# Performance work log

Measured on AMD Instinct MI355X. Metric: run time of the kernel, lower is better.

The kernel has to match this reference:

```python
import jax, jax.numpy as jnp
import numpy as np

M_IND = 1024   # inducing points
K_NN = 16      # nearest neighbors
JITTER = 1e-4


def rbf(X, Z):
    # unit-variance, unit-lengthscale RBF kernel; returns (K, squared distances)
    sq = jnp.sum(X * X, -1)[:, None] + jnp.sum(Z * Z, -1)[None, :] - 2.0 * (X @ Z.T)
    sq = jnp.maximum(sq, 0.0)
    return jnp.exp(-0.5 * sq), sq


def setup_inputs() -> dict:
    key = jax.random.key(0)
    k1, k2, k3 = jax.random.split(key, 3)
    return {
        "X": jax.random.normal(k1, (65536, 3), jnp.float32),
        "Z": jax.random.normal(k2, (M_IND, 3), jnp.float32),
        "Lu_raw": jax.random.normal(k3, (M_IND, M_IND), jnp.float32),
        "mu": jnp.zeros((M_IND,), jnp.float32),
    }


def reference(X, Z, Lu_raw, mu):
    N = X.shape[0]
    Kxx = jnp.ones((N,), X.dtype)                      # diag of RBF(X,X) is 1
    Kxz, dist = rbf(X, Z)                              # [N,M], [N,M]
    Kzz, _ = rbf(Z, Z)                                 # [M,M]

    # transform_to(lower_cholesky): strict lower triangle + exp(diag)
    Lu = jnp.tril(Lu_raw, -1) + jnp.diag(jnp.exp(jnp.diag(Lu_raw)))

    eyeM = jnp.eye(M_IND, dtype=X.dtype)
    L = jnp.linalg.cholesky(Kzz + JITTER * eyeM)       # [M,M]
    Kzz_j = L @ L.T                                    # == little_L @ little_L.T math (Kzz + jitter*I)
    Su = Lu @ Lu.T                                     # full variational covariance

    # K nearest inducing points per data point (argsort(dist)[:, :K])
    _, idx = jax.lax.top_k(-dist, K_NN)                # [N,K]

    lKzz = Kzz_j[idx[:, :, None], idx[:, None, :]]     # [N,K,K] gathered submatrices
    lS = Su[idx[:, :, None], idx[:, None, :]]          # [N,K,K]
    lKxz = jnp.take_along_axis(Kxz, idx, axis=1)       # [N,K]
    lmu = mu[idx]                                      # [N,K]

    eyeK = jnp.eye(K_NN, dtype=X.dtype)
    inv = jnp.linalg.inv(lKzz + JITTER * eyeK)         # batched tiny inverses [N,K,K]
    W = jnp.einsum('nk,nkj->nj', lKxz, inv)            # [N,K]

    mean = jnp.einsum('nk,nk->n', W, lmu)              # [N]
    cov = (Kxx
           - jnp.einsum('ni,nij,nj->n', W, lKzz, W)
           + jnp.einsum('ni,nij,nj->n', W, lS, W))
    std = jnp.sqrt(jnp.clip(cov, 0.05, None))          # qF scale = clamp(cov, 0.05)**0.5
    return jnp.stack([mean, std])                      # [2,N] qF parameters
```

## Files before the change

### kernel.cpp

```cpp
#include <hip/hip_runtime.h>
#include <math.h>

#define N_PTS 65536
#define M_IND 1024
#define KNN 16
#define JITTER 1e-4f

#define PACKED_FLOATS (M_IND * (M_IND + 1) / 2)
#define PACKED_BYTES  ((size_t)PACKED_FLOATS * sizeof(float))

#define TSU 32
#define SU_BLOCKS 528
#define PTS_PER_BLK 128
#define QSTRIDE 17
#define GRID_BLKS (N_PTS / PTS_PER_BLK)

typedef float v2f __attribute__((ext_vector_type(2)));

__device__ __forceinline__ void su_tile(const float* __restrict__ Lu_raw,
                                        float* __restrict__ P,
                                        int bid, int tid,
                                        float (*As)[36], float (*Bs)[36]) {
    int rt = (int)((sqrtf(8.0f * (float)bid + 1.0f) - 1.0f) * 0.5f);
    while ((rt + 1) * (rt + 2) / 2 <= bid) ++rt;
    while (rt * (rt + 1) / 2 > bid) --rt;
    int ct = bid - rt * (rt + 1) / 2;
    int i0 = rt * TSU, j0 = ct * TSU;

    int tx = tid & 15, ty = tid >> 4;
    int sr = tid >> 3, sc = (tid & 7) << 2;
    float a00 = 0.f, a01 = 0.f, a10 = 0.f, a11 = 0.f;

    int nch = ct + 1;
    int gi = i0 + sr, gj = j0 + sr;
    float4 pa = *(const float4*)(Lu_raw + (unsigned)gi * M_IND + sc);
    float4 pb = *(const float4*)(Lu_raw + (unsigned)gj * M_IND + sc);

    for (int c = 0; c < nch; ++c) {
        int gk = (c << 5) + sc;
        float aa[4] = {pa.x, pa.y, pa.z, pa.w};
        float bb[4] = {pb.x, pb.y, pb.z, pb.w};
        #pragma unroll
        for (int q = 0; q < 4; ++q) {
            int k = gk + q;
            aa[q] = (k < gi) ? aa[q] : ((k == gi) ? __expf(aa[q]) : 0.0f);
            bb[q] = (k < gj) ? bb[q] : ((k == gj) ? __expf(bb[q]) : 0.0f);
        }
        *(float4*)&As[sr][sc] = make_float4(aa[0], aa[1], aa[2], aa[3]);
        *(float4*)&Bs[sr][sc] = make_float4(bb[0], bb[1], bb[2], bb[3]);
        __syncthreads();
        if (c + 1 < nch) {
            int kn = ((c + 1) << 5) + sc;
            pa = *(const float4*)(Lu_raw + (unsigned)gi * M_IND + kn);
            pb = *(const float4*)(Lu_raw + (unsigned)gj * M_IND + kn);
        }
        #pragma unroll
        for (int kk = 0; kk < 32; kk += 4) {
            float4 av0 = *(const float4*)&As[ty][kk];
            float4 av1 = *(const float4*)&As[ty + 16][kk];
            float4 bv0 = *(const float4*)&Bs[tx][kk];
            float4 bv1 = *(const float4*)&Bs[tx + 16][kk];
            a00 = fmaf(av0.x, bv0.x, fmaf(av0.y, bv0.y, fmaf(av0.z, bv0.z, fmaf(av0.w, bv0.w, a00))));
            a01 = fmaf(av0.x, bv1.x, fmaf(av0.y, bv1.y, fmaf(av0.z, bv1.z, fmaf(av0.w, bv1.w, a01))));
            a10 = fmaf(av1.x, bv0.x, fmaf(av1.y, bv0.y, fmaf(av1.z, bv0.z, fmaf(av1.w, bv0.w, a10))));
            a11 = fmaf(av1.x, bv1.x, fmaf(av1.y, bv1.y, fmaf(av1.z, bv1.z, fmaf(av1.w, bv1.w, a11))));
        }
        __syncthreads();
    }

    int ia = i0 + ty, ib = i0 + ty + 16;
    int ja = j0 + tx, jb = j0 + tx + 16;
    if (ja <= ia) P[((unsigned)ia * (ia + 1) >> 1) + ja] = a00;
    if (jb <= ia) P[((unsigned)ia * (ia + 1) >> 1) + jb] = a01;
    if (ja <= ib) P[((unsigned)ib * (ib + 1) >> 1) + ja] = a10;
    if (jb <= ib) P[((unsigned)ib * (ib + 1) >> 1) + jb] = a11;
}

__global__ __launch_bounds__(256) void su_kernel(const float* __restrict__ Lu_raw,
                                                 float* __restrict__ P) {
    __shared__ float As[TSU][36];
    __shared__ float Bs[TSU][36];
    su_tile(Lu_raw, P, blockIdx.x, threadIdx.x, As, Bs);
}

__device__ __forceinline__ void ce(unsigned long long& x, unsigned long long& y) {
    unsigned long long a = x, b = y;
    bool c = a < b;
    x = c ? a : b;
    y = c ? b : a;
}
__device__ __forceinline__ void ce(float& x, float& y) {
    float a = fminf(x, y), b = fmaxf(x, y);
    x = a; y = b;
}
__device__ __forceinline__ void ce(v2f& x, v2f& y) {
    v2f a = __builtin_elementwise_min(x, y);
    v2f b = __builtin_elementwise_max(x, y);
    x = a; y = b;
}

template <typename KT>
__device__ __forceinline__ void sort16(KT* a) {
    #pragma unroll
    for (int p = 1; p < 16; p <<= 1)
        #pragma unroll
        for (int k = p; k >= 1; k >>= 1)
            #pragma unroll
            for (int j = k & (p - 1); j + k < 16; j += 2 * k)
                #pragma unroll
                for (int i = 0; i < k; ++i)
                    if (i + j + k < 16)
                        if (((i + j) / (2 * p)) == ((i + j + k) / (2 * p)))
                            ce(a[i + j], a[i + j + k]);
}

template <typename KT>
__device__ __forceinline__ void cleanup16(KT* a) {
    #pragma unroll
    for (int d = 8; d >= 1; d >>= 1)
        #pragma unroll
        for (int i = 0; i < 16; ++i)
            if ((i & d) == 0) ce(a[i], a[i | d]);
}

__device__ __forceinline__ float distf(float4 z, float x0, float x1, float x2, float xq) {
    float dot = fmaf(x0, z.x, fmaf(x1, z.y, x2 * z.z));
    return fmaxf(fmaf(-2.0f, dot, xq + z.w), 0.0f);
}

__device__ __forceinline__ v2f dist2(float4 z, v2f x0, v2f x1, v2f x2, v2f xq) {
    v2f zx = {z.x, z.x}, zy = {z.y, z.y}, zz = {z.z, z.z}, zw = {z.w, z.w};
    v2f dot = __builtin_elementwise_fma(x0, zx,
              __builtin_elementwise_fma(x1, zy, x2 * zz));
    v2f d = __builtin_elementwise_fma((v2f){-2.0f, -2.0f}, dot, xq + zw);
    return __builtin_elementwise_max(d, (v2f){0.0f, 0.0f});
}

__device__ __forceinline__ v2f shfl_xor_v2f(v2f v, int mask) {
    unsigned long long u = __builtin_bit_cast(unsigned long long, v);
    u = __shfl_xor(u, mask, 64);
    return __builtin_bit_cast(v2f, u);
}

template <int MODE>
__global__ __launch_bounds__(256, 2) void vnngp_kernel(const float* __restrict__ X,
                                                       const float* __restrict__ Z,
                                                       const float* __restrict__ mu,
                                                       float* __restrict__ P,
                                                       const float* __restrict__ Lu_raw,
                                                       unsigned int* __restrict__ ctr,
                                                       float* __restrict__ out) {
    __shared__ __align__(16) char smem[37888];
    float4* Zs = (float4*)smem;
    float* mus = (float*)(smem + 16384);
    unsigned long long* qb = (unsigned long long*)(smem + 20480);
    int tid = threadIdx.x;

    for (int r = tid; r < M_IND; r += 256) {
        float zx = Z[r * 3 + 0], zy = Z[r * 3 + 1], zz = Z[r * 3 + 2];
        Zs[r] = make_float4(zx, zy, zz, zx * zx + zy * zy + zz * zz);
        mus[r] = mu[r];
    }

    if (MODE == 2) {
        float (*As)[36] = (float (*)[36])(smem + 20480);
        float (*Bs)[36] = (float (*)[36])(smem + 20480 + 4608);
        for (int t = blockIdx.x; t < SU_BLOCKS; t += GRID_BLKS)
            su_tile(Lu_raw, P, t, tid, As, Bs);
        __syncthreads();
        if (tid == 0) {
            __threadfence();
            atomicAdd(ctr, 1u);
        }
    } else {
        __syncthreads();
    }

    {
        int pt = tid >> 2, sub = tid & 3;
        int nA = blockIdx.x * PTS_PER_BLK + pt;
        int nB = nA + 64;
        float xA0 = X[nA * 3 + 0], xA1 = X[nA * 3 + 1], xA2 = X[nA * 3 + 2];
        float xB0 = X[nB * 3 + 0], xB1 = X[nB * 3 + 1], xB2 = X[nB * 3 + 2];
        v2f x0p = {xA0, xB0}, x1p = {xA1, xB1}, x2p = {xA2, xB2};
        v2f xqp = __builtin_elementwise_fma(x0p, x0p,
                  __builtin_elementwise_fma(x1p, x1p, x2p * x2p));
        int mbase = sub << 8;
        int rot = sub << 1;

        v2f T[16];
        #pragma unroll
        for (int j = 0; j < 16; ++j) T[j] = (v2f){3.4e38f, 3.4e38f};
        #pragma unroll 1
        for (int c = 0; c < 16; ++c) {
            int base = mbase + (c << 4);
            #pragma unroll
            for (int j = 0; j < 16; ++j) {
                int m = base + ((j + rot) & 15);
                v2f d = dist2(Zs[m], x0p, x1p, x2p, xqp);
                T[j] = __builtin_elementwise_min(T[j], d);
            }
        }
        sort16(T);
        #pragma unroll
        for (int round = 1; round <= 2; round <<= 1) {
            v2f o[16];
            #pragma unroll
            for (int i = 0; i < 16; ++i) o[i] = shfl_xor_v2f(T[i], round);
            #pragma unroll
            for (int i = 0; i < 16; ++i)
                T[i] = __builtin_elementwise_min(T[i], o[15 - i]);
            cleanup16(T);
        }
        v2f Tst = T[15];

        unsigned short* mycA = ((unsigned short*)qb) + pt * (QSTRIDE * 4) + sub * 16;
        unsigned short* mycB = ((unsigned short*)qb) + (pt + 64) * (QSTRIDE * 4) + sub * 16;
        int cntA = 0, cntB = 0;
        #pragma unroll 1
        for (int c = 0; c < 16; ++c) {
            int base = mbase + (c << 4);
            #pragma unroll
            for (int j = 0; j < 16; ++j) {
                int m = base + ((j + rot) & 15);
                v2f d = dist2(Zs[m], x0p, x1p, x2p, xqp);
                if (d.x <= Tst.x) { if (cntA < 16) mycA[cntA] = (unsigned short)m; ++cntA; }
                if (d.y <= Tst.y) { if (cntB < 16) mycB[cntB] = (unsigned short)m; ++cntB; }
            }
        }

        int ovfA = cntA > 16 ? 1 : 0;
        ovfA |= __shfl_xor(ovfA, 1, 64);
        ovfA |= __shfl_xor(ovfA, 2, 64);
        int ovfB = cntB > 16 ? 1 : 0;
        ovfB |= __shfl_xor(ovfB, 1, 64);
        ovfB |= __shfl_xor(ovfB, 2, 64);

        float xqA = xqp.x, xqB = xqp.y;

        if (!ovfA) {
            const unsigned long long* m64 = (const unsigned long long*)mycA;
            unsigned long long raw[4] = {m64[0], m64[1], m64[2], m64[3]};
            unsigned long long C[16];
            #pragma unroll
            for (int i = 0; i < 16; ++i) {
                int m = (int)((raw[i >> 2] >> ((i & 3) * 16)) & 0x3FF);
                float d = distf(Zs[m], xA0, xA1, xA2, xqA);
                unsigned long long key =
                    ((unsigned long long)__float_as_uint(d) << 32) | (unsigned)m;
                C[i] = (i < cntA) ? key : ~0ULL;
            }
            sort16(C);
            #pragma unroll
            for (int round = 1; round <= 2; round <<= 1) {
                unsigned long long o[16];
                #pragma unroll
                for (int i = 0; i < 16; ++i) o[i] = __shfl_xor(C[i], round, 64);
                #pragma unroll
                for (int i = 0; i < 16; ++i) {
                    unsigned long long b = o[15 - i];
                    C[i] = C[i] < b ? C[i] : b;
                }
                cleanup16(C);
            }
            if (sub == 0) {
                #pragma unroll
                for (int i = 0; i < 16; ++i) qb[pt * QSTRIDE + i] = C[i];
            }
        } else if (sub == 0) {
            unsigned long long R[16];
            #pragma unroll
            for (int i = 0; i < 16; ++i) R[i] = ~0ULL;
            for (int m = 0; m < M_IND; ++m) {
                float d = distf(Zs[m], xA0, xA1, xA2, xqA);
                unsigned long long kk =
                    ((unsigned long long)__float_as_uint(d) << 32) | (unsigned)m;
                if (kk < R[15]) {
                    #pragma unroll
                    for (int j = 0; j < 16; ++j) {
                        unsigned long long t = R[j];
                        bool cc = kk < t;
                        R[j] = cc ? kk : t;
                        kk = cc ? t : kk;
                    }
                }
            }
            #pragma unroll
            for (int i = 0; i < 16; ++i) qb[pt * QSTRIDE + i] = R[i];
        }

        if (!ovfB) {
            const unsigned long long* m64 = (const unsigned long long*)mycB;
            unsigned long long raw[4] = {m64[0], m64[1], m64[2], m64[3]};
            unsigned long long C[16];
            #pragma unroll
            for (int i = 0; i < 16; ++i) {
                int m = (int)((raw[i >> 2] >> ((i & 3) * 16)) & 0x3FF);
                float d = distf(Zs[m], xB0, xB1, xB2, xqB);
                unsigned long long key =
                    ((unsigned long long)__float_as_uint(d) << 32) | (unsigned)m;
                C[i] = (i < cntB) ? key : ~0ULL;
            }
            sort16(C);
            #pragma unroll
            for (int round = 1; round <= 2; round <<= 1) {
                unsigned long long o[16];
                #pragma unroll
                for (int i = 0; i < 16; ++i) o[i] = __shfl_xor(C[i], round, 64);
                #pragma unroll
                for (int i = 0; i < 16; ++i) {
                    unsigned long long b = o[15 - i];
                    C[i] = C[i] < b ? C[i] : b;
                }
                cleanup16(C);
            }
            if (sub == 0) {
                #pragma unroll
                for (int i = 0; i < 16; ++i) qb[(pt + 64) * QSTRIDE + i] = C[i];
            }
        } else if (sub == 0) {
            unsigned long long R[16];
            #pragma unroll
            for (int i = 0; i < 16; ++i) R[i] = ~0ULL;
            for (int m = 0; m < M_IND; ++m) {
                float d = distf(Zs[m], xB0, xB1, xB2, xqB);
                unsigned long long kk =
                    ((unsigned long long)__float_as_uint(d) << 32) | (unsigned)m;
                if (kk < R[15]) {
                    #pragma unroll
                    for (int j = 0; j < 16; ++j) {
                        unsigned long long t = R[j];
                        bool cc = kk < t;
                        R[j] = cc ? kk : t;
                        kk = cc ? t : kk;
                    }
                }
            }
            #pragma unroll
            for (int i = 0; i < 16; ++i) qb[(pt + 64) * QSTRIDE + i] = R[i];
        }
    }
    __syncthreads();

    if (MODE == 2) {
        if (tid == 0) {
            while (__hip_atomic_load(ctr, __ATOMIC_ACQUIRE, __HIP_MEMORY_SCOPE_AGENT)
                   < (unsigned)GRID_BLKS)
                __builtin_amdgcn_s_sleep(8);
        }
        __syncthreads();
    }
    if (tid >= PTS_PER_BLK) return;

    int n = blockIdx.x * PTS_PER_BLK + tid;
    int idx[KNN];
    float kv[KNN];
    float nx[KNN], ny[KNN], nz[KNN], nq[KNN];
    #pragma unroll
    for (int a = 0; a < KNN; ++a) {
        unsigned long long k = qb[tid * QSTRIDE + a];
        idx[a] = (int)(k & 0xFFFFFFFFULL);
        float d = __uint_as_float((unsigned)(k >> 32));
        kv[a] = __expf(-0.5f * d);
        float4 z = Zs[idx[a]];
        nx[a] = z.x; ny[a] = z.y; nz[a] = z.z; nq[a] = z.w;
    }

    float A[KNN * (KNN + 1) / 2];
    #pragma unroll
    for (int r = 0; r < KNN; ++r) {
        A[r * (r + 1) / 2 + r] = 1.0f + 2.0f * JITTER;
        #pragma unroll
        for (int c = 0; c < r; ++c) {
            float dd = nq[r] + nq[c]
                     - 2.0f * (nx[r] * nx[c] + ny[r] * ny[c] + nz[r] * nz[c]);
            dd = fmaxf(dd, 0.0f);
            A[r * (r + 1) / 2 + c] = __expf(-0.5f * dd);
        }
    }

    #pragma unroll
    for (int c = 0; c < KNN; ++c) {
        float diag = A[c * (c + 1) / 2 + c];
        #pragma unroll
        for (int k = 0; k < c; ++k) {
            float l = A[c * (c + 1) / 2 + k];
            diag = fmaf(-l, l, diag);
        }
        float s = sqrtf(fmaxf(diag, 1e-12f));
        float rinv = 1.0f / s;
        A[c * (c + 1) / 2 + c] = rinv;
        #pragma unroll
        for (int r = c + 1; r < KNN; ++r) {
            float v = A[r * (r + 1) / 2 + c];
            #pragma unroll
            for (int k = 0; k < c; ++k)
                v = fmaf(-A[r * (r + 1) / 2 + k], A[c * (c + 1) / 2 + k], v);
            A[r * (r + 1) / 2 + c] = v * rinv;
        }
    }

    float w[KNN];
    #pragma unroll
    for (int r = 0; r < KNN; ++r) {
        float v = kv[r];
        #pragma unroll
        for (int c = 0; c < r; ++c) v = fmaf(-A[r * (r + 1) / 2 + c], w[c], v);
        w[r] = v * A[r * (r + 1) / 2 + r];
    }
    #pragma unroll
    for (int r = KNN - 1; r >= 0; --r) {
        float v = w[r];
        #pragma unroll
        for (int c = r + 1; c < KNN; ++c) v = fmaf(-A[c * (c + 1) / 2 + r], w[c], v);
        w[r] = v * A[r * (r + 1) / 2 + r];
    }

    float wk = 0.f, ww = 0.f, mean = 0.f;
    #pragma unroll
    for (int a = 0; a < KNN; ++a) {
        wk = fmaf(w[a], kv[a], wk);
        ww = fmaf(w[a], w[a], ww);
        mean = fmaf(w[a], mus[idx[a]], mean);
    }

    float qs = 0.f;
    if (MODE != 0) {
        #pragma unroll
        for (int r = 0; r < KNN; ++r) {
            int a = idx[r];
            float wr = w[r];
            float rowacc = 0.f;
            #pragma unroll
            for (int c = 0; c < r; ++c) {
                int b = idx[c];
                int hi = a > b ? a : b;
                int lo = a > b ? b : a;
                rowacc = fmaf(w[c], P[((unsigned)hi * (hi + 1) >> 1) + lo], rowacc);
            }
            qs = fmaf(wr, fmaf(wr, P[((unsigned)a * (a + 1) >> 1) + a], 2.0f * rowacc), qs);
        }
    } else {
        int si[KNN]; float sw[KNN];
        #pragma unroll
        for (int a = 0; a < KNN; ++a) { si[a] = idx[a]; sw[a] = w[a]; }
        #pragma unroll
        for (int a = 1; a < KNN; ++a) {
            int iv = si[a]; float wv = sw[a];
            int b = a - 1;
            while (b >= 0 && si[b] > iv) { si[b + 1] = si[b]; sw[b + 1] = sw[b]; --b; }
            si[b + 1] = iv; sw[b + 1] = wv;
        }
        int s = 0;
        int kend = si[KNN - 1];
        for (int k = 0; k <= kend; ++k) {
            float v = 0.f;
            if (s < KNN && si[s] == k) {
                v = sw[s] * __expf(Lu_raw[(unsigned)k * M_IND + k]);
                ++s;
            }
            for (int a = s; a < KNN; ++a)
                v = fmaf(sw[a], Lu_raw[(unsigned)si[a] * M_IND + k], v);
            qs = fmaf(v, v, qs);
        }
    }

    float cov = 1.0f - (wk - JITTER * ww) + qs;
    float sd = sqrtf(fmaxf(cov, 0.05f));
    out[n] = mean;
    out[N_PTS + n] = sd;
}

extern "C" void kernel_launch(void* const* d_in, const int* in_sizes, int n_in,
                              void* d_out, int out_size, void* d_ws, size_t ws_size,
                              hipStream_t stream) {
    const float* X      = (const float*)d_in[0];
    const float* Z      = (const float*)d_in[1];
    const float* Lu_raw = (const float*)d_in[2];
    const float* mu     = (const float*)d_in[3];
    float* out = (float*)d_out;

    if (ws_size >= PACKED_BYTES + 64) {
        float* P = (float*)d_ws;
        unsigned int* ctr = (unsigned int*)((char*)d_ws + PACKED_BYTES);
        hipMemsetAsync(ctr, 0, sizeof(unsigned int), stream);
        vnngp_kernel<2><<<GRID_BLKS, 256, 0, stream>>>(X, Z, mu, P, Lu_raw, ctr, out);
    } else if (ws_size >= PACKED_BYTES) {
        float* P = (float*)d_ws;
        su_kernel<<<SU_BLOCKS, 256, 0, stream>>>(Lu_raw, P);
        vnngp_kernel<1><<<GRID_BLKS, 256, 0, stream>>>(X, Z, mu, P, Lu_raw, nullptr, out);
    } else {
        vnngp_kernel<0><<<GRID_BLKS, 256, 0, stream>>>(X, Z, mu, nullptr, Lu_raw, nullptr, out);
    }
}
```

Baseline: 173.3 us.

## Split KNN search over eight lanes with four points per thread group

The top-16 search now runs eight lanes per group of four query points, each lane scanning 128 inducing points, in place of four lanes per two points each scanning 256. Distances are computed for four points per Z load, which amortises shared-memory reads, and the threshold merge gains a third shuffle round. Per-lane candidate buffers shrink to 12 entries, so the serial fallback is taken more often, and QSTRIDE and shared memory grow to make room. The Su tile assignment is also remapped so each block does one tile, with the first 16 blocks doing one extra.

After: 191.5 us. 1.1x slower.

```diff
diff --git a/kernel.cpp b/kernel.cpp
--- a/kernel.cpp
+++ b/kernel.cpp
@@ -12,7 +12,7 @@
 #define TSU 32
 #define SU_BLOCKS 528
 #define PTS_PER_BLK 128
-#define QSTRIDE 17
+#define QSTRIDE 25
 #define GRID_BLKS (N_PTS / PTS_PER_BLK)
 
 typedef float v2f __attribute__((ext_vector_type(2)));
@@ -89,10 +89,6 @@
     x = c ? a : b;
     y = c ? b : a;
 }
-__device__ __forceinline__ void ce(float& x, float& y) {
-    float a = fminf(x, y), b = fmaxf(x, y);
-    x = a; y = b;
-}
 __device__ __forceinline__ void ce(v2f& x, v2f& y) {
     v2f a = __builtin_elementwise_min(x, y);
     v2f b = __builtin_elementwise_max(x, y);
@@ -128,18 +124,50 @@
     return fmaxf(fmaf(-2.0f, dot, xq + z.w), 0.0f);
 }
 
-__device__ __forceinline__ v2f dist2(float4 z, v2f x0, v2f x1, v2f x2, v2f xq) {
+__device__ __forceinline__ void dist4(float4 z,
+                                      v2f x0a, v2f x1a, v2f x2a, v2f xqa,
+                                      v2f x0b, v2f x1b, v2f x2b, v2f xqb,
+                                      v2f& da, v2f& db) {
     v2f zx = {z.x, z.x}, zy = {z.y, z.y}, zz = {z.z, z.z}, zw = {z.w, z.w};
-    v2f dot = __builtin_elementwise_fma(x0, zx,
-              __builtin_elementwise_fma(x1, zy, x2 * zz));
-    v2f d = __builtin_elementwise_fma((v2f){-2.0f, -2.0f}, dot, xq + zw);
-    return __builtin_elementwise_max(d, (v2f){0.0f, 0.0f});
+    v2f m2 = {-2.0f, -2.0f}, z0 = {0.0f, 0.0f};
+    v2f dota = __builtin_elementwise_fma(x0a, zx,
+               __builtin_elementwise_fma(x1a, zy, x2a * zz));
+    da = __builtin_elementwise_max(
+        __builtin_elementwise_fma(m2, dota, xqa + zw), z0);
+    v2f dotb = __builtin_elementwise_fma(x0b, zx,
+               __builtin_elementwise_fma(x1b, zy, x2b * zz));
+    db = __builtin_elementwise_max(
+        __builtin_elementwise_fma(m2, dotb, xqb + zw), z0);
 }
 
 __device__ __forceinline__ v2f shfl_xor_v2f(v2f v, int mask) {
     unsigned long long u = __builtin_bit_cast(unsigned long long, v);
     u = __shfl_xor(u, mask, 64);
     return __builtin_bit_cast(v2f, u);
+}
+
+__device__ __forceinline__ void serial_knn(const float4* Zs, float x0, float x1,
+                                           float x2, float xq,
+                                           unsigned long long* dst) {
+    unsigned long long R[16];
+    #pragma unroll
+    for (int i = 0; i < 16; ++i) R[i] = ~0ULL;
+    for (int m = 0; m < M_IND; ++m) {
+        float d = distf(Zs[m], x0, x1, x2, xq);
+        unsigned long long kk =
+            ((unsigned long long)__float_as_uint(d) << 32) | (unsigned)m;
+        if (kk < R[15]) {
+            #pragma unroll
+            for (int j = 0; j < 16; ++j) {
+                unsigned long long t = R[j];
+                bool cc = kk < t;
+                R[j] = cc ? kk : t;
+                kk = cc ? t : kk;
+            }
+        }
+    }
+    #pragma unroll
+    for (int i = 0; i < 16; ++i) dst[i] = R[i];
 }
 
 template <int MODE>
@@ -150,7 +178,7 @@
                                                        const float* __restrict__ Lu_raw,
                                                        unsigned int* __restrict__ ctr,
                                                        float* __restrict__ out) {
-    __shared__ __align__(16) char smem[37888];
+    __shared__ __align__(16) char smem[46080];
     float4* Zs = (float4*)smem;
     float* mus = (float*)(smem + 16384);
     unsigned long long* qb = (unsigned long long*)(smem + 20480);
@@ -165,8 +193,17 @@
     if (MODE == 2) {
         float (*As)[36] = (float (*)[36])(smem + 20480);
         float (*Bs)[36] = (float (*)[36])(smem + 20480 + 4608);
-        for (int t = blockIdx.x; t < SU_BLOCKS; t += GRID_BLKS)
-            su_tile(Lu_raw, P, t, tid, As, Bs);
+        int t = blockIdx.x;
+        #pragma unroll
+        for (int r = 16; r < 32; ++r) {
+            int s = (r * (r + 1)) >> 1;
+            if (t >= s) ++t;
+        }
+        su_tile(Lu_raw, P, t, tid, As, Bs);
+        if (blockIdx.x < 16) {
+            int r = 16 + blockIdx.x;
+            su_tile(Lu_raw, P, (r * (r + 1)) >> 1, tid, As, Bs);
+        }
         __syncthreads();
         if (tid == 0) {
             __threadfence();
@@ -177,167 +214,119 @@
     }
 
     {
-        int pt = tid >> 2, sub = tid & 3;
-        int nA = blockIdx.x * PTS_PER_BLK + pt;
-        int nB = nA + 64;
-        float xA0 = X[nA * 3 + 0], xA1 = X[nA * 3 + 1], xA2 = X[nA * 3 + 2];
-        float xB0 = X[nB * 3 + 0], xB1 = X[nB * 3 + 1], xB2 = X[nB * 3 + 2];
-        v2f x0p = {xA0, xB0}, x1p = {xA1, xB1}, x2p = {xA2, xB2};
-        v2f xqp = __builtin_elementwise_fma(x0p, x0p,
-                  __builtin_elementwise_fma(x1p, x1p, x2p * x2p));
-        int mbase = sub << 8;
-        int rot = sub << 1;
-
-        v2f T[16];
-        #pragma unroll
-        for (int j = 0; j < 16; ++j) T[j] = (v2f){3.4e38f, 3.4e38f};
+        int g = tid >> 3, sub = tid & 7;
+        int nbase = blockIdx.x * PTS_PER_BLK + g;
+        float xs[4][3];
+        #pragma unroll
+        for (int q = 0; q < 4; ++q) {
+            int n = nbase + q * 32;
+            xs[q][0] = X[n * 3 + 0]; xs[q][1] = X[n * 3 + 1]; xs[q][2] = X[n * 3 + 2];
+        }
+        v2f x0a = {xs[0][0], xs[1][0]}, x1a = {xs[0][1], xs[1][1]}, x2a = {xs[0][2], xs[1][2]};
+        v2f x0b = {xs[2][0], xs[3][0]}, x1b = {xs[2][1], xs[3][1]}, x2b = {xs[2][2], xs[3][2]};
+        v2f xqa = __builtin_elementwise_fma(x0a, x0a,
+                  __builtin_elementwise_fma(x1a, x1a, x2a * x2a));
+        v2f xqb = __builtin_elementwise_fma(x0b, x0b,
+                  __builtin_elementwise_fma(x1b, x1b, x2b * x2b));
+        int mbase = sub << 7;
+        int rot = sub;
+
+        v2f Ta[16], Tb[16];
+        #pragma unroll
+        for (int j = 0; j < 16; ++j) { Ta[j] = (v2f){3.4e38f, 3.4e38f}; Tb[j] = Ta[j]; }
         #pragma unroll 1
-        for (int c = 0; c < 16; ++c) {
+        for (int c = 0; c < 8; ++c) {
             int base = mbase + (c << 4);
             #pragma unroll
             for (int j = 0; j < 16; ++j) {
                 int m = base + ((j + rot) & 15);
-                v2f d = dist2(Zs[m], x0p, x1p, x2p, xqp);
-                T[j] = __builtin_elementwise_min(T[j], d);
-            }
-        }
-        sort16(T);
-        #pragma unroll
-        for (int round = 1; round <= 2; round <<= 1) {
-            v2f o[16];
-            #pragma unroll
-            for (int i = 0; i < 16; ++i) o[i] = shfl_xor_v2f(T[i], round);
-            #pragma unroll
-            for (int i = 0; i < 16; ++i)
-                T[i] = __builtin_elementwise_min(T[i], o[15 - i]);
-            cleanup16(T);
-        }
-        v2f Tst = T[15];
-
-        unsigned short* mycA = ((unsigned short*)qb) + pt * (QSTRIDE * 4) + sub * 16;
-        unsigned short* mycB = ((unsigned short*)qb) + (pt + 64) * (QSTRIDE * 4) + sub * 16;
-        int cntA = 0, cntB = 0;
+                v2f da, db;
+                dist4(Zs[m], x0a, x1a, x2a, xqa, x0b, x1b, x2b, xqb, da, db);
+                Ta[j] = __builtin_elementwise_min(Ta[j], da);
+                Tb[j] = __builtin_elementwise_min(Tb[j], db);
+            }
+        }
+        sort16(Ta);
+        sort16(Tb);
+        #pragma unroll
+        for (int round = 1; round <= 4; round <<= 1) {
+            v2f oa[16], ob[16];
+            #pragma unroll
+            for (int i = 0; i < 16; ++i) {
+                oa[i] = shfl_xor_v2f(Ta[i], round);
+                ob[i] = shfl_xor_v2f(Tb[i], round);
+            }
+            #pragma unroll
+            for (int i = 0; i < 16; ++i) {
+                Ta[i] = __builtin_elementwise_min(Ta[i], oa[15 - i]);
+                Tb[i] = __builtin_elementwise_min(Tb[i], ob[15 - i]);
+            }
+            cleanup16(Ta);
+            cleanup16(Tb);
+        }
+        v2f Tsta = Ta[15], Tstb = Tb[15];
+
+        unsigned short* myc[4];
+        int cnt[4] = {0, 0, 0, 0};
+        #pragma unroll
+        for (int q = 0; q < 4; ++q)
+            myc[q] = ((unsigned short*)qb) + (g + q * 32) * (QSTRIDE * 4) + sub * 12;
         #pragma unroll 1
-        for (int c = 0; c < 16; ++c) {
+        for (int c = 0; c < 8; ++c) {
             int base = mbase + (c << 4);
             #pragma unroll
             for (int j = 0; j < 16; ++j) {
                 int m = base + ((j + rot) & 15);
-                v2f d = dist2(Zs[m], x0p, x1p, x2p, xqp);
-                if (d.x <= Tst.x) { if (cntA < 16) mycA[cntA] = (unsigned short)m; ++cntA; }
-                if (d.y <= Tst.y) { if (cntB < 16) mycB[cntB] = (unsigned short)m; ++cntB; }
-            }
-        }
-
-        int ovfA = cntA > 16 ? 1 : 0;
-        ovfA |= __shfl_xor(ovfA, 1, 64);
-        ovfA |= __shfl_xor(ovfA, 2, 64);
-        int ovfB = cntB > 16 ? 1 : 0;
-        ovfB |= __shfl_xor(ovfB, 1, 64);
-        ovfB |= __shfl_xor(ovfB, 2, 64);
-
-        float xqA = xqp.x, xqB = xqp.y;
-
-        if (!ovfA) {
-            const unsigned long long* m64 = (const unsigned long long*)mycA;
-            unsigned long long raw[4] = {m64[0], m64[1], m64[2], m64[3]};
-            unsigned long long C[16];
-            #pragma unroll
-            for (int i = 0; i < 16; ++i) {
-                int m = (int)((raw[i >> 2] >> ((i & 3) * 16)) & 0x3FF);
-                float d = distf(Zs[m], xA0, xA1, xA2, xqA);
-                unsigned long long key =
-                    ((unsigned long long)__float_as_uint(d) << 32) | (unsigned)m;
-                C[i] = (i < cntA) ? key : ~0ULL;
-            }
-            sort16(C);
-            #pragma unroll
-            for (int round = 1; round <= 2; round <<= 1) {
-                unsigned long long o[16];
-                #pragma unroll
-                for (int i = 0; i < 16; ++i) o[i] = __shfl_xor(C[i], round, 64);
+                v2f da, db;
+                dist4(Zs[m], x0a, x1a, x2a, xqa, x0b, x1b, x2b, xqb, da, db);
+                if (da.x <= Tsta.x) { if (cnt[0] < 12) myc[0][cnt[0]] = (unsigned short)m; ++cnt[0]; }
+                if (da.y <= Tsta.y) { if (cnt[1] < 12) myc[1][cnt[1]] = (unsigned short)m; ++cnt[1]; }
+                if (db.x <= Tstb.x) { if (cnt[2] < 12) myc[2][cnt[2]] = (unsigned short)m; ++cnt[2]; }
+                if (db.y <= Tstb.y) { if (cnt[3] < 12) myc[3][cnt[3]] = (unsigned short)m; ++cnt[3]; }
+            }
+        }
+
+        #pragma unroll 1
+        for (int q = 0; q < 4; ++q) {
+            int p = g + q * 32;
+            int ovf = cnt[q] > 12 ? 1 : 0;
+            ovf |= __shfl_xor(ovf, 1, 64);
+            ovf |= __shfl_xor(ovf, 2, 64);
+            ovf |= __shfl_xor(ovf, 4, 64);
+            float px0 = xs[q][0], px1 = xs[q][1], px2 = xs[q][2];
+            float pxq = (q == 0) ? xqa.x : (q == 1) ? xqa.y : (q == 2) ? xqb.x : xqb.y;
+            if (!ovf) {
+                const unsigned long long* m64 = (const unsigned long long*)myc[q];
+                unsigned long long raw[3] = {m64[0], m64[1], m64[2]};
+                unsigned long long C[16];
                 #pragma unroll
                 for (int i = 0; i < 16; ++i) {
-                    unsigned long long b = o[15 - i];
-                    C[i] = C[i] < b ? C[i] : b;
+                    int m = (i < 12) ? (int)((raw[i >> 2] >> ((i & 3) * 16)) & 0x3FF) : 0;
+                    float d = distf(Zs[m], px0, px1, px2, pxq);
+                    unsigned long long key =
+                        ((unsigned long long)__float_as_uint(d) << 32) | (unsigned)m;
+                    C[i] = (i < cnt[q]) ? key : ~0ULL;
                 }
-                cleanup16(C);
-            }
-            if (sub == 0) {
+                sort16(C);
                 #pragma unroll
-                for (int i = 0; i < 16; ++i) qb[pt * QSTRIDE + i] = C[i];
-            }
-        } else if (sub == 0) {
-            unsigned long long R[16];
-            #pragma unroll
-            for (int i = 0; i < 16; ++i) R[i] = ~0ULL;
-            for (int m = 0; m < M_IND; ++m) {
-                float d = distf(Zs[m], xA0, xA1, xA2, xqA);
-                unsigned long long kk =
-                    ((unsigned long long)__float_as_uint(d) << 32) | (unsigned)m;
-                if (kk < R[15]) {
+                for (int round = 1; round <= 4; round <<= 1) {
+                    unsigned long long o[16];
                     #pragma unroll
-                    for (int j = 0; j < 16; ++j) {
-                        unsigned long long t = R[j];
-                        bool cc = kk < t;
-                        R[j] = cc ? kk : t;
-                        kk = cc ? t : kk;
+                    for (int i = 0; i < 16; ++i) o[i] = __shfl_xor(C[i], round, 64);
+                    #pragma unroll
+                    for (int i = 0; i < 16; ++i) {
+                        unsigned long long b = o[15 - i];
+                        C[i] = C[i] < b ? C[i] : b;
                     }
+                    cleanup16(C);
                 }
-            }
-            #pragma unroll
-            for (int i = 0; i < 16; ++i) qb[pt * QSTRIDE + i] = R[i];
-        }
-
-        if (!ovfB) {
-            const unsigned long long* m64 = (const unsigned long long*)mycB;
-            unsigned long long raw[4] = {m64[0], m64[1], m64[2], m64[3]};
-            unsigned long long C[16];
-            #pragma unroll
-            for (int i = 0; i < 16; ++i) {
-                int m = (int)((raw[i >> 2] >> ((i & 3) * 16)) & 0x3FF);
-                float d = distf(Zs[m], xB0, xB1, xB2, xqB);
-                unsigned long long key =
-                    ((unsigned long long)__float_as_uint(d) << 32) | (unsigned)m;
-                C[i] = (i < cntB) ? key : ~0ULL;
-            }
-            sort16(C);
-            #pragma unroll
-            for (int round = 1; round <= 2; round <<= 1) {
-                unsigned long long o[16];
-                #pragma unroll
-                for (int i = 0; i < 16; ++i) o[i] = __shfl_xor(C[i], round, 64);
-                #pragma unroll
-                for (int i = 0; i < 16; ++i) {
-                    unsigned long long b = o[15 - i];
-                    C[i] = C[i] < b ? C[i] : b;
+                if (sub == 0) {
+                    #pragma unroll
+                    for (int i = 0; i < 16; ++i) qb[p * QSTRIDE + i] = C[i];
                 }
-                cleanup16(C);
-            }
-            if (sub == 0) {
-                #pragma unroll
-                for (int i = 0; i < 16; ++i) qb[(pt + 64) * QSTRIDE + i] = C[i];
-            }
-        } else if (sub == 0) {
-            unsigned long long R[16];
-            #pragma unroll
-            for (int i = 0; i < 16; ++i) R[i] = ~0ULL;
-            for (int m = 0; m < M_IND; ++m) {
-                float d = distf(Zs[m], xB0, xB1, xB2, xqB);
-                unsigned long long kk =
-                    ((unsigned long long)__float_as_uint(d) << 32) | (unsigned)m;
-                if (kk < R[15]) {
-                    #pragma unroll
-                    for (int j = 0; j < 16; ++j) {
-                        unsigned long long t = R[j];
-                        bool cc = kk < t;
-                        R[j] = cc ? kk : t;
-                        kk = cc ? t : kk;
-                    }
-                }
-            }
-            #pragma unroll
-            for (int i = 0; i < 16; ++i) qb[(pt + 64) * QSTRIDE + i] = R[i];
+            } else if (sub == 0) {
+                serial_knn(Zs, px0, px1, px2, pxq, &qb[p * QSTRIDE]);
+            }
         }
     }
     __syncthreads();
```
